# Kernel tuning notes

Measured on AMD Instinct MI355X. Metric: run time of the kernel, lower is better.

The kernel has to match this reference:

```python
import jax, jax.numpy as jnp
import numpy as np

HID = 256  # hidden_dim in the torch module


def _graph_conv(h, edges, W0, b0, W1, b1):
    # pytorch3d.ops.GraphConv (undirected): out = w0(h) + sum_{neighbors} w1(h_nbr),
    # where each edge (i, j) contributes in both directions.
    out = h @ W0 + b0          # [V, H]
    nbr = h @ W1 + b1          # [V, H]
    i, j = edges[:, 0], edges[:, 1]
    out = out.at[i].add(nbr[j])
    out = out.at[j].add(nbr[i])
    return out


def setup_inputs() -> dict:
    key = jax.random.key(0)
    ks = jax.random.split(key, 16)
    V, E, F, H = 20496, 61440, 3840, HID  # 8 meshes x (2562 verts, 7680 edges); F = 256+512+1024+2048

    def w(k, shape):
        return jax.random.normal(k, shape, dtype=jnp.float32) * 0.02

    return {
        "vert_img_feats": jax.random.normal(ks[0], (V, F), dtype=jnp.float32),
        "verts": jax.random.normal(ks[1], (V, 3), dtype=jnp.float32),
        "edges": jax.random.randint(ks[2], (E, 2), 0, V),
        # bottleneck Linear(3840 -> 256)
        "Wb": w(ks[3], (F, H)), "bb": jnp.zeros((H,), jnp.float32),
        # GraphConv 0: input_dim = 3 + 256
        "W0_0": w(ks[4], (3 + H, H)), "b0_0": jnp.zeros((H,), jnp.float32),
        "W1_0": w(ks[5], (3 + H, H)), "b1_0": jnp.zeros((H,), jnp.float32),
        # GraphConv 1..9 stacked
        "gW0": w(ks[6], (9, H, H)), "gb0": jnp.zeros((9, H), jnp.float32),
        "gW1": w(ks[7], (9, H, H)), "gb1": jnp.zeros((9, H), jnp.float32),
        # vert_offset Linear(256 -> 3)
        "Wo": w(ks[8], (H, 3)), "bo": jnp.zeros((3,), jnp.float32),
        # asym_conf MLP: 256 -> 256 -> 64 -> 32 -> 1
        "A1": w(ks[9], (H, H)), "a1": jnp.zeros((H,), jnp.float32),
        "A2": w(ks[10], (H, 64)), "a2": jnp.zeros((64,), jnp.float32),
        "A3": w(ks[11], (64, 32)), "a3": jnp.zeros((32,), jnp.float32),
        "A4": w(ks[12], (32, 1)), "a4": jnp.zeros((1,), jnp.float32),
    }


def reference(vert_img_feats, verts, edges, Wb, bb, W0_0, b0_0, W1_0, b1_0,
              gW0, gb0, gW1, gb1, Wo, bo, A1, a1, A2, a2, A3, a3, A4, a4):
    # bottleneck + ReLU on per-vertex image features (vert_align output)
    h_img = jax.nn.relu(vert_img_feats @ Wb + bb)            # [V, 256]
    h = jnp.concatenate([h_img, verts], axis=1)              # [V, 259]
    h = jax.nn.relu(_graph_conv(h, edges, W0_0, b0_0, W1_0, b1_0))
    for k in range(9):  # fixed layer count, structurally distinct params
        h = jax.nn.relu(_graph_conv(h, edges, gW0[k], gb0[k], gW1[k], gb1[k]))
    delta_v = h @ Wo + bo                                    # [V, 3]
    z = jax.nn.relu(h @ A1 + a1)
    z = jax.nn.relu(z @ A2 + a2)
    z = jax.nn.relu(z @ A3 + a3)
    asym_conf = jax.nn.sigmoid(z @ A4 + a4)                  # [V, 1]
    return delta_v, asym_conf
```

## Files before the change

kernel.cpp:

```cpp
#include <hip/hip_runtime.h>

typedef _Float16 half8  __attribute__((ext_vector_type(8)));
typedef _Float16 half4v __attribute__((ext_vector_type(4)));
typedef float    floatx4 __attribute__((ext_vector_type(4)));

#define DEVINL __device__ __forceinline__

DEVINL void async_cp16(const void* g, void* l){
  __builtin_amdgcn_global_load_lds(
      (const __attribute__((address_space(1))) void*)g,
      (__attribute__((address_space(3))) void*)l,
      16, 0, 0);
}

DEVINL float wred64(float x){
  #pragma unroll
  for (int m = 32; m; m >>= 1) x += __shfl_xor(x, m, 64);
  return x;
}

__global__ __launch_bounds__(256) void k_gemm_bb(
    const float* __restrict__ A, const _Float16* __restrict__ BT,
    const float* __restrict__ bias, _Float16* __restrict__ C,
    int M, int K, int lda)
{
  constexpr int BM = 128, BN = 128, BK = 32;
  __shared__ alignas(16) float    As[BM * BK];
  __shared__ alignas(16) _Float16 Bs[BN * BK];
  const int tid = threadIdx.x, wid = tid >> 6, lane = tid & 63;
  const int bm = blockIdx.x, bn = blockIdx.y;

  const float* aSrc[4]; float* aDst[4];
  const int uSw = (lane & 7) ^ ((lane >> 3) & 7);
  #pragma unroll
  for (int c = 0; c < 4; c++){
    int rloc = wid * 32 + c * 8 + (lane >> 3);
    int r = min(bm * BM + rloc, M - 1);
    aSrc[c] = A + (size_t)r * lda + uSw * 4;
    aDst[c] = &As[(wid * 32 + c * 8) * BK];
  }
  const _Float16* bSrc[2]; _Float16* bDst[2];
  #pragma unroll
  for (int s = 0; s < 2; s++){
    int rb = bn * BN + (wid * 2 + s) * 16 + (lane >> 2);
    bSrc[s] = BT + (size_t)rb * K + (lane & 3) * 8;
    bDst[s] = &Bs[(wid * 2 + s) * 16 * BK];
  }

  floatx4 acc[4][4];
  #pragma unroll
  for (int mt = 0; mt < 4; mt++)
    #pragma unroll
    for (int nt = 0; nt < 4; nt++) acc[mt][nt] = {0.f, 0.f, 0.f, 0.f};

  const int arow0 = (wid >> 1) * 64 + (lane & 15);
  const int g2 = (lane >> 4) * 2;
  const int boff = ((wid & 1) * 64 + (lane & 15)) * BK + (lane >> 4) * 8;

  for (int k0 = 0; k0 < K; k0 += BK){
    __syncthreads();
    #pragma unroll
    for (int c = 0; c < 4; c++) async_cp16(aSrc[c] + k0, aDst[c]);
    #pragma unroll
    for (int s = 0; s < 2; s++) async_cp16(bSrc[s] + k0, bDst[s]);
    __syncthreads();
    half8 af[4], bf[4];
    #pragma unroll
    for (int mt = 0; mt < 4; mt++){
      int arow = arow0 + mt * 16;
      int a7 = arow & 7;
      floatx4 lo = *(const floatx4*)&As[arow * BK + ((g2    ) ^ a7) * 4];
      floatx4 hi = *(const floatx4*)&As[arow * BK + ((g2 + 1) ^ a7) * 4];
      #pragma unroll
      for (int j = 0; j < 4; j++){ af[mt][j] = (_Float16)lo[j]; af[mt][4+j] = (_Float16)hi[j]; }
    }
    #pragma unroll
    for (int nt = 0; nt < 4; nt++) bf[nt] = *(const half8*)&Bs[boff + nt * 16 * BK];
    #pragma unroll
    for (int mt = 0; mt < 4; mt++)
      #pragma unroll
      for (int nt = 0; nt < 4; nt++)
        acc[mt][nt] = __builtin_amdgcn_mfma_f32_16x16x32_f16(af[mt], bf[nt], acc[mt][nt], 0, 0, 0);
  }

  const int colLocal = (wid & 1) * 64 + (lane & 15);
  const int rowLocal = (wid >> 1) * 64 + (lane >> 4) * 4;
  #pragma unroll
  for (int nt = 0; nt < 4; nt++){
    int col = bn * BN + colLocal + nt * 16;
    float b = bias[col];
    #pragma unroll
    for (int mt = 0; mt < 4; mt++){
      int r0 = bm * BM + rowLocal + mt * 16;
      #pragma unroll
      for (int i = 0; i < 4; i++){
        int r = r0 + i;
        if (r < M){
          float v = fmaxf(acc[mt][nt][i] + b, 0.f);
          C[(size_t)r * 256 + col] = (_Float16)v;
        }
      }
    }
  }
}

template<bool RELU, bool SPLIT, bool VERTC>
__global__ __launch_bounds__(256) void k_gemm_h(
    const _Float16* __restrict__ A, int Mstore, int Vreal,
    const _Float16* __restrict__ BT,
    const float* __restrict__ bias0, const float* __restrict__ bias1,
    const float* __restrict__ vertW, const float* __restrict__ verts,
    _Float16* __restrict__ C0, _Float16* __restrict__ C1)
{
  constexpr int BM = 128, BN = 128, BK = 32, K = 256;
  __shared__ alignas(16) _Float16 As[BM * BK];
  __shared__ alignas(16) _Float16 Bs[BN * BK];
  const int tid = threadIdx.x, wid = tid >> 6, lane = tid & 63;
  const int bm = blockIdx.x, bn = blockIdx.y;
  const int sub = lane >> 2, kof = (lane & 3) * 8;

  const _Float16* aSrc[2]; _Float16* aDst[2];
  const _Float16* bSrc[2]; _Float16* bDst[2];
  #pragma unroll
  for (int s = 0; s < 2; s++){
    int r = bm * BM + (wid * 2 + s) * 16 + sub;
    aSrc[s] = A + (size_t)r * K + kof;
    aDst[s] = &As[(wid * 2 + s) * 512];
    int rb = bn * BN + (wid * 2 + s) * 16 + sub;
    bSrc[s] = BT + (size_t)rb * K + kof;
    bDst[s] = &Bs[(wid * 2 + s) * 512];
  }

  floatx4 acc[4][4];
  #pragma unroll
  for (int mt = 0; mt < 4; mt++)
    #pragma unroll
    for (int nt = 0; nt < 4; nt++) acc[mt][nt] = {0.f, 0.f, 0.f, 0.f};

  const int aoff = ((wid >> 1) * 64 + (lane & 15)) * BK + (lane >> 4) * 8;
  const int boff = ((wid & 1) * 64 + (lane & 15)) * BK + (lane >> 4) * 8;

  for (int k0 = 0; k0 < K; k0 += BK){
    __syncthreads();
    async_cp16(aSrc[0] + k0, aDst[0]);
    async_cp16(aSrc[1] + k0, aDst[1]);
    async_cp16(bSrc[0] + k0, bDst[0]);
    async_cp16(bSrc[1] + k0, bDst[1]);
    __syncthreads();
    half8 af[4], bf[4];
    #pragma unroll
    for (int mt = 0; mt < 4; mt++) af[mt] = *(const half8*)&As[aoff + mt * 16 * BK];
    #pragma unroll
    for (int nt = 0; nt < 4; nt++) bf[nt] = *(const half8*)&Bs[boff + nt * 16 * BK];
    #pragma unroll
    for (int mt = 0; mt < 4; mt++)
      #pragma unroll
      for (int nt = 0; nt < 4; nt++)
        acc[mt][nt] = __builtin_amdgcn_mfma_f32_16x16x32_f16(af[mt], bf[nt], acc[mt][nt], 0, 0, 0);
  }

  const int colLocal = (wid & 1) * 64 + (lane & 15);
  const int rowLocal = (wid >> 1) * 64 + (lane >> 4) * 4;
  #pragma unroll
  for (int nt = 0; nt < 4; nt++){
    int g = bn * BN + colLocal + nt * 16;
    _Float16* Cp = C0;
    const float* bp = bias0;
    int col = g;
    if (SPLIT && g >= 256){ Cp = C1; bp = bias1; col = g - 256; }
    float b = bp[col];
    float w0 = 0.f, w1 = 0.f, w2 = 0.f;
    if (VERTC){ w0 = vertW[g*3+0]; w1 = vertW[g*3+1]; w2 = vertW[g*3+2]; }
    #pragma unroll
    for (int mt = 0; mt < 4; mt++){
      int r0 = bm * BM + rowLocal + mt * 16;
      #pragma unroll
      for (int i = 0; i < 4; i++){
        int r = r0 + i;
        if (r < Mstore){
          float v = acc[mt][nt][i] + b;
          if (VERTC){
            int vr = min(r, Vreal - 1);
            v += verts[vr*3+0] * w0 + verts[vr*3+1] * w1 + verts[vr*3+2] * w2;
          }
          if (RELU) v = fmaxf(v, 0.f);
          Cp[(size_t)r * 256 + col] = (_Float16)v;
        }
      }
    }
  }
}

__global__ __launch_bounds__(256) void k_fill(const int* __restrict__ e, int E,
                                              int* __restrict__ cnt, int* __restrict__ adj){
  int t = blockIdx.x * 256 + threadIdx.x;
  if (t >= E) return;
  int i = e[t*2], j = e[t*2+1];
  int s = atomicAdd(&cnt[i], 1); if (s < 64) adj[(size_t)i*64 + s] = j;
  int q = atomicAdd(&cnt[j], 1); if (q < 64) adj[(size_t)j*64 + q] = i;
}

__global__ __launch_bounds__(256) void k_pack(
    const float* __restrict__ Wb,
    const float* __restrict__ W0_0, const float* __restrict__ W1_0,
    const float* __restrict__ gW0,  const float* __restrict__ gW1,
    const float* __restrict__ A1,
    _Float16* __restrict__ WbT, _Float16* __restrict__ convB,
    _Float16* __restrict__ A1T, float* __restrict__ vertW)
{
  const int S1 = 256*3840, S2 = 10*512*256, S3 = 256*256, S4 = 512*3;
  int id = blockIdx.x * 256 + threadIdx.x;
  if (id < S1){ int n = id / 3840, k = id % 3840; WbT[id] = (_Float16)Wb[(size_t)k*256 + n]; return; }
  id -= S1;
  if (id < S2){
    int l = id / (512*256); int rem = id % (512*256);
    int r = rem / 256, k = rem % 256;
    const float* W0 = (l == 0) ? W0_0 : gW0 + (size_t)(l-1)*65536;
    const float* W1 = (l == 0) ? W1_0 : gW1 + (size_t)(l-1)*65536;
    convB[id] = (_Float16)((r < 256) ? W0[(size_t)k*256 + r] : W1[(size_t)k*256 + (r-256)]);
    return;
  }
  id -= S2;
  if (id < S3){ int n = id / 256, k = id % 256; A1T[id] = (_Float16)A1[(size_t)k*256 + n]; return; }
  id -= S3;
  if (id < S4){
    int n = id / 3, c = id % 3;
    vertW[id] = (n < 256) ? W0_0[(size_t)(256+c)*256 + n]
                          : W1_0[(size_t)(256+c)*256 + (n-256)];
  }
}

__global__ __launch_bounds__(256) void k_gather(
    const _Float16* __restrict__ outB, const _Float16* __restrict__ nbrB,
    const int* __restrict__ cnt, const int* __restrict__ adj,
    _Float16* __restrict__ h, int V)
{
  int gw = (int)((blockIdx.x * 256 + threadIdx.x) >> 6);
  int lane = threadIdx.x & 63;
  if (gw >= V) return;
  half4v o = ((const half4v*)(outB + (size_t)gw * 256))[lane];
  float a0 = (float)o[0], a1 = (float)o[1], a2 = (float)o[2], a3 = (float)o[3];
  int n = min(cnt[gw], 64);
  const int* ap = adj + (size_t)gw * 64;
  for (int d = 0; d < n; d++){
    int u = ap[d];
    half4v x = ((const half4v*)(nbrB + (size_t)u * 256))[lane];
    a0 += (float)x[0]; a1 += (float)x[1]; a2 += (float)x[2]; a3 += (float)x[3];
  }
  half4v rr;
  rr[0] = (_Float16)fmaxf(a0, 0.f); rr[1] = (_Float16)fmaxf(a1, 0.f);
  rr[2] = (_Float16)fmaxf(a2, 0.f); rr[3] = (_Float16)fmaxf(a3, 0.f);
  ((half4v*)(h + (size_t)gw * 256))[lane] = rr;
}

__global__ __launch_bounds__(1024) void k_head(
    const _Float16* __restrict__ hA, const _Float16* __restrict__ z1,
    const float* __restrict__ Wo, const float* __restrict__ bo,
    const float* __restrict__ A2, const float* __restrict__ a2,
    const float* __restrict__ A3, const float* __restrict__ a3,
    const float* __restrict__ A4, const float* __restrict__ a4,
    float* __restrict__ dOut, int V)
{
  __shared__ float A2s[256 * 64];
  __shared__ float A3s[64 * 32];
  __shared__ float Wos[768];
  __shared__ float zrow[16][256];
  __shared__ float z2s[16][64];
  const int tid = threadIdx.x;
  for (int i = tid; i < 256*64; i += 1024) A2s[i] = A2[i];
  for (int i = tid; i < 64*32;  i += 1024) A3s[i] = A3[i];
  if (tid < 768) Wos[tid] = Wo[tid];
  __syncthreads();
  const int wid = tid >> 6, lane = tid & 63;
  const int v = blockIdx.x * 16 + wid;
  if (v >= V) return;

  half4v hv = ((const half4v*)(hA + (size_t)v * 256))[lane];
  float hf[4] = { (float)hv[0], (float)hv[1], (float)hv[2], (float)hv[3] };
  float p0 = 0.f, p1 = 0.f, p2 = 0.f;
  int c0 = lane * 4;
  #pragma unroll
  for (int j = 0; j < 4; j++){
    p0 += hf[j] * Wos[(c0+j)*3 + 0];
    p1 += hf[j] * Wos[(c0+j)*3 + 1];
    p2 += hf[j] * Wos[(c0+j)*3 + 2];
  }
  p0 = wred64(p0); p1 = wred64(p1); p2 = wred64(p2);
  if (lane == 0){
    dOut[(size_t)v*3 + 0] = p0 + bo[0];
    dOut[(size_t)v*3 + 1] = p1 + bo[1];
    dOut[(size_t)v*3 + 2] = p2 + bo[2];
  }

  half4v zv = ((const half4v*)(z1 + (size_t)v * 256))[lane];
  floatx4 zf; zf[0] = (float)zv[0]; zf[1] = (float)zv[1]; zf[2] = (float)zv[2]; zf[3] = (float)zv[3];
  ((floatx4*)zrow[wid])[lane] = zf;
  __threadfence_block();
  float acc2 = a2[lane];
  #pragma unroll 4
  for (int c = 0; c < 256; c++) acc2 += zrow[wid][c] * A2s[c*64 + lane];
  acc2 = fmaxf(acc2, 0.f);
  z2s[wid][lane] = acc2;
  __threadfence_block();
  int o = lane & 31;
  float acc3 = a3[o];
  #pragma unroll 4
  for (int c = 0; c < 64; c++) acc3 += z2s[wid][c] * A3s[c*32 + o];
  acc3 = fmaxf(acc3, 0.f);
  float p = (lane < 32) ? acc3 * A4[lane] : 0.f;
  p = wred64(p);
  if (lane == 0){
    float s = 1.f / (1.f + expf(-(p + a4[0])));
    dOut[(size_t)V*3 + v] = s;
  }
}

extern "C" void kernel_launch(void* const* d_in, const int* in_sizes, int n_in,
                              void* d_out, int out_size, void* d_ws, size_t ws_size,
                              hipStream_t stream)
{
  const int V = 20496, E = 61440, F = 3840, Vpad = 20608;
  const float* X     = (const float*)d_in[0];
  const float* verts = (const float*)d_in[1];
  const int*   edges = (const int*)d_in[2];
  const float* Wb    = (const float*)d_in[3];
  const float* bb    = (const float*)d_in[4];
  const float* W0_0  = (const float*)d_in[5];
  const float* b0_0  = (const float*)d_in[6];
  const float* W1_0  = (const float*)d_in[7];
  const float* b1_0  = (const float*)d_in[8];
  const float* gW0   = (const float*)d_in[9];
  const float* gb0   = (const float*)d_in[10];
  const float* gW1   = (const float*)d_in[11];
  const float* gb1   = (const float*)d_in[12];
  const float* Wo    = (const float*)d_in[13];
  const float* bo    = (const float*)d_in[14];
  const float* A1    = (const float*)d_in[15];
  const float* a1    = (const float*)d_in[16];
  const float* A2    = (const float*)d_in[17];
  const float* a2    = (const float*)d_in[18];
  const float* A3    = (const float*)d_in[19];
  const float* a3    = (const float*)d_in[20];
  const float* A4    = (const float*)d_in[21];
  const float* a4    = (const float*)d_in[22];

  char* w = (char*)d_ws;
  const size_t SA = (size_t)Vpad * 256 * 2;
  _Float16* hA    = (_Float16*)(w);
  _Float16* outB  = (_Float16*)(w + SA);
  _Float16* nbrB  = (_Float16*)(w + 2*SA);
  _Float16* z1    = (_Float16*)(w + 3*SA);
  size_t off = 4 * SA;
  _Float16* WbT   = (_Float16*)(w + off); off += (size_t)256*3840*2;
  _Float16* convB = (_Float16*)(w + off); off += (size_t)10*512*256*2;
  _Float16* A1T   = (_Float16*)(w + off); off += (size_t)256*256*2;
  float*    vertW = (float*)(w + off);    off += (size_t)512*3*4;
  int*      cnt   = (int*)(w + off);      off += (size_t)V*4;
  int*      adj   = (int*)(w + off);

  hipMemsetAsync(cnt, 0, (size_t)V*4, stream);
  hipMemsetAsync(hA + (size_t)V*256, 0, (size_t)(Vpad - V)*256*2, stream);

  k_fill<<<dim3((E + 255)/256), dim3(256), 0, stream>>>(edges, E, cnt, adj);
  {
    const int total = 256*3840 + 10*512*256 + 256*256 + 512*3;
    k_pack<<<dim3((total + 255)/256), dim3(256), 0, stream>>>(
        Wb, W0_0, W1_0, gW0, gW1, A1, WbT, convB, A1T, vertW);
  }

  k_gemm_bb<<<dim3(161, 2), dim3(256), 0, stream>>>(X, WbT, bb, hA, V, F, F);

  for (int l = 0; l < 10; l++){
    const float* bp0 = l ? gb0 + (size_t)(l-1)*256 : b0_0;
    const float* bp1 = l ? gb1 + (size_t)(l-1)*256 : b1_0;
    const _Float16* Bt = convB + (size_t)l * 512 * 256;
    if (l == 0)
      k_gemm_h<false, true, true><<<dim3(161, 4), dim3(256), 0, stream>>>(
          hA, Vpad, V, Bt, bp0, bp1, vertW, verts, outB, nbrB);
    else
      k_gemm_h<false, true, false><<<dim3(161, 4), dim3(256), 0, stream>>>(
          hA, Vpad, V, Bt, bp0, bp1, nullptr, nullptr, outB, nbrB);
    k_gather<<<dim3(5124), dim3(256), 0, stream>>>(outB, nbrB, cnt, adj, hA, V);
  }

  k_gemm_h<true, false, false><<<dim3(161, 2), dim3(256), 0, stream>>>(
      hA, Vpad, V, A1T, a1, nullptr, nullptr, nullptr, z1, nullptr);

  k_head<<<dim3(V/16), dim3(1024), 0, stream>>>(
      hA, z1, Wo, bo, A2, a2, A3, a3, A4, a4, (float*)d_out, V);
}
```

Before: 1.070 ms.

## Split-K bottleneck GEMM, fragment-packed conv weights, tiled transpose, unrolled gather

The bottleneck GEMM is split along K into four chunks that write fp32 partials, and a separate reduce kernel adds bias, applies ReLU and zeroes the padding rows. This raises parallelism above the 322 blocks the grid had before. Conv and head GEMMs now preload a whole 128-column weight panel, packed into MFMA fragment order, into LDS once, and read A straight from global memory, which removes the per-K-step barriers. Weight packing is split into a tiled LDS transpose and a fragment packer, and the neighbor gather loop is unrolled by two. The cost is extra fp32 partial traffic and 64KB of LDS per block, which can lower occupancy.

```diff
diff --git a/kernel.cpp b/kernel.cpp
--- a/kernel.cpp
+++ b/kernel.cpp
@@ -21,29 +21,30 @@
 
 __global__ __launch_bounds__(256) void k_gemm_bb(
     const float* __restrict__ A, const _Float16* __restrict__ BT,
-    const float* __restrict__ bias, _Float16* __restrict__ C,
-    int M, int K, int lda)
-{
-  constexpr int BM = 128, BN = 128, BK = 32;
+    float* __restrict__ P, int M, int Mpad, int K, int lda, int kChunk)
+{
+  constexpr int BM = 128, BK = 32;
   __shared__ alignas(16) float    As[BM * BK];
-  __shared__ alignas(16) _Float16 Bs[BN * BK];
+  __shared__ alignas(16) _Float16 Bs[BM * BK];
   const int tid = threadIdx.x, wid = tid >> 6, lane = tid & 63;
-  const int bm = blockIdx.x, bn = blockIdx.y;
+  const int bm = blockIdx.x, bn = blockIdx.y, bz = blockIdx.z;
+  const int kbeg = bz * kChunk, kend = kbeg + kChunk;
 
   const float* aSrc[4]; float* aDst[4];
-  const int uSw = (lane & 7) ^ ((lane >> 3) & 7);
+  const int uSwA = (lane & 7) ^ ((lane >> 3) & 7);
   #pragma unroll
   for (int c = 0; c < 4; c++){
     int rloc = wid * 32 + c * 8 + (lane >> 3);
     int r = min(bm * BM + rloc, M - 1);
-    aSrc[c] = A + (size_t)r * lda + uSw * 4;
+    aSrc[c] = A + (size_t)r * lda + uSwA * 4;
     aDst[c] = &As[(wid * 32 + c * 8) * BK];
   }
   const _Float16* bSrc[2]; _Float16* bDst[2];
+  const int uSwB = (lane & 3) ^ ((lane >> 2) & 3);
   #pragma unroll
   for (int s = 0; s < 2; s++){
-    int rb = bn * BN + (wid * 2 + s) * 16 + (lane >> 2);
-    bSrc[s] = BT + (size_t)rb * K + (lane & 3) * 8;
+    int rb = bn * BM + (wid * 2 + s) * 16 + (lane >> 2);
+    bSrc[s] = BT + (size_t)rb * K + uSwB * 8;
     bDst[s] = &Bs[(wid * 2 + s) * 16 * BK];
   }
 
@@ -55,9 +56,11 @@
 
   const int arow0 = (wid >> 1) * 64 + (lane & 15);
   const int g2 = (lane >> 4) * 2;
-  const int boff = ((wid & 1) * 64 + (lane & 15)) * BK + (lane >> 4) * 8;
-
-  for (int k0 = 0; k0 < K; k0 += BK){
+  const int a7 = lane & 7;
+  const int brow0 = (wid & 1) * 64 + (lane & 15);
+  const int ub = (lane >> 4) ^ (lane & 3);
+
+  for (int k0 = kbeg; k0 < kend; k0 += BK){
     __syncthreads();
     #pragma unroll
     for (int c = 0; c < 4; c++) async_cp16(aSrc[c] + k0, aDst[c]);
@@ -68,14 +71,14 @@
     #pragma unroll
     for (int mt = 0; mt < 4; mt++){
       int arow = arow0 + mt * 16;
-      int a7 = arow & 7;
       floatx4 lo = *(const floatx4*)&As[arow * BK + ((g2    ) ^ a7) * 4];
       floatx4 hi = *(const floatx4*)&As[arow * BK + ((g2 + 1) ^ a7) * 4];
       #pragma unroll
       for (int j = 0; j < 4; j++){ af[mt][j] = (_Float16)lo[j]; af[mt][4+j] = (_Float16)hi[j]; }
     }
     #pragma unroll
-    for (int nt = 0; nt < 4; nt++) bf[nt] = *(const half8*)&Bs[boff + nt * 16 * BK];
+    for (int nt = 0; nt < 4; nt++)
+      bf[nt] = *(const half8*)&Bs[(brow0 + nt * 16) * BK + ub * 8];
     #pragma unroll
     for (int mt = 0; mt < 4; mt++)
       #pragma unroll
@@ -85,51 +88,72 @@
 
   const int colLocal = (wid & 1) * 64 + (lane & 15);
   const int rowLocal = (wid >> 1) * 64 + (lane >> 4) * 4;
+  float* Pz = P + (size_t)bz * Mpad * 256;
   #pragma unroll
   for (int nt = 0; nt < 4; nt++){
-    int col = bn * BN + colLocal + nt * 16;
-    float b = bias[col];
+    int col = bn * BM + colLocal + nt * 16;
     #pragma unroll
     for (int mt = 0; mt < 4; mt++){
       int r0 = bm * BM + rowLocal + mt * 16;
       #pragma unroll
-      for (int i = 0; i < 4; i++){
-        int r = r0 + i;
-        if (r < M){
-          float v = fmaxf(acc[mt][nt][i] + b, 0.f);
-          C[(size_t)r * 256 + col] = (_Float16)v;
-        }
-      }
+      for (int i = 0; i < 4; i++)
+        Pz[(size_t)(r0 + i) * 256 + col] = acc[mt][nt][i];
     }
   }
 }
 
+__global__ __launch_bounds__(256) void k_reduce(
+    const float* __restrict__ P, const float* __restrict__ bias,
+    _Float16* __restrict__ hA, int V, int Mpad)
+{
+  int idx = blockIdx.x * 256 + threadIdx.x;
+  int base = idx * 4;
+  int r = base >> 8, c = base & 255;
+  const size_t stride = (size_t)Mpad * 256;
+  const float* p = P + (size_t)r * 256 + c;
+  floatx4 s0 = *(const floatx4*)(p);
+  floatx4 s1 = *(const floatx4*)(p + stride);
+  floatx4 s2 = *(const floatx4*)(p + 2 * stride);
+  floatx4 s3 = *(const floatx4*)(p + 3 * stride);
+  floatx4 b = *(const floatx4*)(bias + c);
+  half4v o;
+  if (r < V){
+    #pragma unroll
+    for (int e = 0; e < 4; e++)
+      o[e] = (_Float16)fmaxf(s0[e] + s1[e] + s2[e] + s3[e] + b[e], 0.f);
+  } else {
+    #pragma unroll
+    for (int e = 0; e < 4; e++) o[e] = (_Float16)0.f;
+  }
+  *(half4v*)(hA + (size_t)r * 256 + c) = o;
+}
+
 template<bool RELU, bool SPLIT, bool VERTC>
-__global__ __launch_bounds__(256) void k_gemm_h(
-    const _Float16* __restrict__ A, int Mstore, int Vreal,
-    const _Float16* __restrict__ BT,
+__global__ __launch_bounds__(256) void k_conv(
+    const _Float16* __restrict__ A,
+    const _Float16* __restrict__ BTfrag,
     const float* __restrict__ bias0, const float* __restrict__ bias1,
     const float* __restrict__ vertW, const float* __restrict__ verts,
-    _Float16* __restrict__ C0, _Float16* __restrict__ C1)
-{
-  constexpr int BM = 128, BN = 128, BK = 32, K = 256;
-  __shared__ alignas(16) _Float16 As[BM * BK];
-  __shared__ alignas(16) _Float16 Bs[BN * BK];
+    _Float16* __restrict__ C0, _Float16* __restrict__ C1, int Vreal)
+{
+  __shared__ alignas(16) _Float16 Bs[32768];
   const int tid = threadIdx.x, wid = tid >> 6, lane = tid & 63;
   const int bm = blockIdx.x, bn = blockIdx.y;
-  const int sub = lane >> 2, kof = (lane & 3) * 8;
-
-  const _Float16* aSrc[2]; _Float16* aDst[2];
-  const _Float16* bSrc[2]; _Float16* bDst[2];
-  #pragma unroll
-  for (int s = 0; s < 2; s++){
-    int r = bm * BM + (wid * 2 + s) * 16 + sub;
-    aSrc[s] = A + (size_t)r * K + kof;
-    aDst[s] = &As[(wid * 2 + s) * 512];
-    int rb = bn * BN + (wid * 2 + s) * 16 + sub;
-    bSrc[s] = BT + (size_t)rb * K + kof;
-    bDst[s] = &Bs[(wid * 2 + s) * 512];
-  }
+
+  const _Float16* src = BTfrag + (size_t)bn * 32768;
+  #pragma unroll
+  for (int jj = 0; jj < 16; jj++){
+    int e = (jj * 256 + tid) * 8;
+    *(half8*)&Bs[e] = *(const half8*)&src[e];
+  }
+  __syncthreads();
+
+  const _Float16* Arow[4];
+  #pragma unroll
+  for (int mt = 0; mt < 4; mt++)
+    Arow[mt] = A + (size_t)(bm * 128 + (wid >> 1) * 64 + mt * 16 + (lane & 15)) * 256
+                 + (lane >> 4) * 8;
+  const int nbase = (wid & 1) * 4;
 
   floatx4 acc[4][4];
   #pragma unroll
@@ -137,21 +161,14 @@
     #pragma unroll
     for (int nt = 0; nt < 4; nt++) acc[mt][nt] = {0.f, 0.f, 0.f, 0.f};
 
-  const int aoff = ((wid >> 1) * 64 + (lane & 15)) * BK + (lane >> 4) * 8;
-  const int boff = ((wid & 1) * 64 + (lane & 15)) * BK + (lane >> 4) * 8;
-
-  for (int k0 = 0; k0 < K; k0 += BK){
-    __syncthreads();
-    async_cp16(aSrc[0] + k0, aDst[0]);
-    async_cp16(aSrc[1] + k0, aDst[1]);
-    async_cp16(bSrc[0] + k0, bDst[0]);
-    async_cp16(bSrc[1] + k0, bDst[1]);
-    __syncthreads();
+  #pragma unroll
+  for (int j = 0; j < 8; j++){
     half8 af[4], bf[4];
     #pragma unroll
-    for (int mt = 0; mt < 4; mt++) af[mt] = *(const half8*)&As[aoff + mt * 16 * BK];
-    #pragma unroll
-    for (int nt = 0; nt < 4; nt++) bf[nt] = *(const half8*)&Bs[boff + nt * 16 * BK];
+    for (int mt = 0; mt < 4; mt++) af[mt] = *(const half8*)(Arow[mt] + j * 32);
+    #pragma unroll
+    for (int nt = 0; nt < 4; nt++)
+      bf[nt] = *(const half8*)&Bs[(((nbase + nt) * 8 + j) * 64 + lane) * 8];
     #pragma unroll
     for (int mt = 0; mt < 4; mt++)
       #pragma unroll
@@ -163,7 +180,7 @@
   const int rowLocal = (wid >> 1) * 64 + (lane >> 4) * 4;
   #pragma unroll
   for (int nt = 0; nt < 4; nt++){
-    int g = bn * BN + colLocal + nt * 16;
+    int g = bn * 128 + colLocal + nt * 16;
     _Float16* Cp = C0;
     const float* bp = bias0;
     int col = g;
@@ -173,19 +190,17 @@
     if (VERTC){ w0 = vertW[g*3+0]; w1 = vertW[g*3+1]; w2 = vertW[g*3+2]; }
     #pragma unroll
     for (int mt = 0; mt < 4; mt++){
-      int r0 = bm * BM + rowLocal + mt * 16;
+      int r0 = bm * 128 + rowLocal + mt * 16;
       #pragma unroll
       for (int i = 0; i < 4; i++){
         int r = r0 + i;
-        if (r < Mstore){
-          float v = acc[mt][nt][i] + b;
-          if (VERTC){
-            int vr = min(r, Vreal - 1);
-            v += verts[vr*3+0] * w0 + verts[vr*3+1] * w1 + verts[vr*3+2] * w2;
-          }
-          if (RELU) v = fmaxf(v, 0.f);
-          Cp[(size_t)r * 256 + col] = (_Float16)v;
+        float v = acc[mt][nt][i] + b;
+        if (VERTC){
+          int vr = min(r, Vreal - 1);
+          v += verts[vr*3+0] * w0 + verts[vr*3+1] * w1 + verts[vr*3+2] * w2;
         }
+        if (RELU) v = fmaxf(v, 0.f);
+        Cp[(size_t)r * 256 + col] = (_Float16)v;
       }
     }
   }
@@ -200,33 +215,63 @@
   int q = atomicAdd(&cnt[j], 1); if (q < 64) adj[(size_t)j*64 + q] = i;
 }
 
-__global__ __launch_bounds__(256) void k_pack(
-    const float* __restrict__ Wb,
+__global__ __launch_bounds__(256) void k_trans_bb(
+    const float* __restrict__ Wb, _Float16* __restrict__ WbT)
+{
+  __shared__ float T[64][65];
+  const int k0 = blockIdx.x * 64, n0 = blockIdx.y * 64;
+  const int tr = threadIdx.x >> 6, tc = threadIdx.x & 63;
+  #pragma unroll
+  for (int i = 0; i < 16; i++){
+    int rr = i * 4 + tr;
+    T[rr][tc] = Wb[(size_t)(k0 + rr) * 256 + n0 + tc];
+  }
+  __syncthreads();
+  #pragma unroll
+  for (int i = 0; i < 16; i++){
+    int rr = i * 4 + tr;
+    WbT[(size_t)(n0 + rr) * 3840 + k0 + tc] = (_Float16)T[tc][rr];
+  }
+}
+
+__global__ __launch_bounds__(256) void k_pack_frag(
     const float* __restrict__ W0_0, const float* __restrict__ W1_0,
     const float* __restrict__ gW0,  const float* __restrict__ gW1,
     const float* __restrict__ A1,
-    _Float16* __restrict__ WbT, _Float16* __restrict__ convB,
-    _Float16* __restrict__ A1T, float* __restrict__ vertW)
-{
-  const int S1 = 256*3840, S2 = 10*512*256, S3 = 256*256, S4 = 512*3;
-  int id = blockIdx.x * 256 + threadIdx.x;
-  if (id < S1){ int n = id / 3840, k = id % 3840; WbT[id] = (_Float16)Wb[(size_t)k*256 + n]; return; }
-  id -= S1;
-  if (id < S2){
-    int l = id / (512*256); int rem = id % (512*256);
-    int r = rem / 256, k = rem % 256;
-    const float* W0 = (l == 0) ? W0_0 : gW0 + (size_t)(l-1)*65536;
-    const float* W1 = (l == 0) ? W1_0 : gW1 + (size_t)(l-1)*65536;
-    convB[id] = (_Float16)((r < 256) ? W0[(size_t)k*256 + r] : W1[(size_t)k*256 + (r-256)]);
+    _Float16* __restrict__ convB, _Float16* __restrict__ A1T,
+    float* __restrict__ vertW)
+{
+  if (blockIdx.x == 672){
+    for (int i = threadIdx.x; i < 1536; i += 256){
+      int n = i / 3, c = i % 3;
+      vertW[i] = (n < 256) ? W0_0[(size_t)(256 + c) * 256 + n]
+                           : W1_0[(size_t)(256 + c) * 256 + (n - 256)];
+    }
     return;
   }
-  id -= S2;
-  if (id < S3){ int n = id / 256, k = id % 256; A1T[id] = (_Float16)A1[(size_t)k*256 + n]; return; }
-  id -= S3;
-  if (id < S4){
-    int n = id / 3, c = id % 3;
-    vertW[id] = (n < 256) ? W0_0[(size_t)(256+c)*256 + n]
-                          : W1_0[(size_t)(256+c)*256 + (n-256)];
+  const int gw = blockIdx.x * 4 + (threadIdx.x >> 6);
+  const int lane = threadIdx.x & 63;
+  if (gw < 2560){
+    int L = gw >> 8;
+    int r = gw & 255;
+    int n = (r >> 3) * 16 + (lane & 15);
+    int k = (r & 7) * 32 + (lane >> 4) * 8;
+    const float* W0 = L ? gW0 + (size_t)(L - 1) * 65536 : W0_0;
+    const float* W1 = L ? gW1 + (size_t)(L - 1) * 65536 : W1_0;
+    const float* Wsel = (n < 256) ? W0 : W1;
+    int nn = n & 255;
+    half8 v;
+    #pragma unroll
+    for (int e = 0; e < 8; e++) v[e] = (_Float16)Wsel[(size_t)(k + e) * 256 + nn];
+    *(half8*)&convB[(size_t)L * 131072 + (size_t)r * 512 + lane * 8] = v;
+  } else {
+    int r = gw - 2560;
+    int n = (r >> 3) * 16 + (lane & 15);
+    int k = (r & 7) * 32 + (lane >> 4) * 8;
+    half8 v;
+    #pragma unroll
+    for (int e = 0; e < 8; e++) v[e] = (_Float16)A1[(size_t)(k + e) * 256 + n];
+    *(half8*)&A1T[(size_t)r * 512 + lane * 8] = v;
   }
 }
 
@@ -242,7 +287,15 @@
   float a0 = (float)o[0], a1 = (float)o[1], a2 = (float)o[2], a3 = (float)o[3];
   int n = min(cnt[gw], 64);
   const int* ap = adj + (size_t)gw * 64;
-  for (int d = 0; d < n; d++){
+  int d = 0;
+  for (; d + 1 < n; d += 2){
+    int u0 = ap[d], u1 = ap[d+1];
+    half4v x = ((const half4v*)(nbrB + (size_t)u0 * 256))[lane];
+    half4v y = ((const half4v*)(nbrB + (size_t)u1 * 256))[lane];
+    a0 += (float)x[0] + (float)y[0]; a1 += (float)x[1] + (float)y[1];
+    a2 += (float)x[2] + (float)y[2]; a3 += (float)x[3] + (float)y[3];
+  }
+  if (d < n){
     int u = ap[d];
     half4v x = ((const half4v*)(nbrB + (size_t)u * 256))[lane];
     a0 += (float)x[0]; a1 += (float)x[1]; a2 += (float)x[2]; a3 += (float)x[3];
@@ -324,7 +377,7 @@
   const float* verts = (const float*)d_in[1];
   const int*   edges = (const int*)d_in[2];
   const float* Wb    = (const float*)d_in[3];
-  const float* bb    = (const float*)d_in[4];
+  const float* bbias = (const float*)d_in[4];
   const float* W0_0  = (const float*)d_in[5];
   const float* b0_0  = (const float*)d_in[6];
   const float* W1_0  = (const float*)d_in[7];
@@ -351,40 +404,39 @@
   _Float16* nbrB  = (_Float16*)(w + 2*SA);
   _Float16* z1    = (_Float16*)(w + 3*SA);
   size_t off = 4 * SA;
+  float*    P     = (float*)(w + off);    off += (size_t)4 * Vpad * 256 * 4;
   _Float16* WbT   = (_Float16*)(w + off); off += (size_t)256*3840*2;
-  _Float16* convB = (_Float16*)(w + off); off += (size_t)10*512*256*2;
-  _Float16* A1T   = (_Float16*)(w + off); off += (size_t)256*256*2;
-  float*    vertW = (float*)(w + off);    off += (size_t)512*3*4;
+  _Float16* convB = (_Float16*)(w + off); off += (size_t)10*131072*2;
+  _Float16* A1T   = (_Float16*)(w + off); off += (size_t)131072*2;
+  float*    vertW = (float*)(w + off);    off += (size_t)1536*4;
   int*      cnt   = (int*)(w + off);      off += (size_t)V*4;
   int*      adj   = (int*)(w + off);
 
   hipMemsetAsync(cnt, 0, (size_t)V*4, stream);
-  hipMemsetAsync(hA + (size_t)V*256, 0, (size_t)(Vpad - V)*256*2, stream);
 
   k_fill<<<dim3((E + 255)/256), dim3(256), 0, stream>>>(edges, E, cnt, adj);
-  {
-    const int total = 256*3840 + 10*512*256 + 256*256 + 512*3;
-    k_pack<<<dim3((total + 255)/256), dim3(256), 0, stream>>>(
-        Wb, W0_0, W1_0, gW0, gW1, A1, WbT, convB, A1T, vertW);
-  }
-
-  k_gemm_bb<<<dim3(161, 2), dim3(256), 0, stream>>>(X, WbT, bb, hA, V, F, F);
+  k_trans_bb<<<dim3(60, 4), dim3(256), 0, stream>>>(Wb, WbT);
+  k_pack_frag<<<dim3(673), dim3(256), 0, stream>>>(
+      W0_0, W1_0, gW0, gW1, A1, convB, A1T, vertW);
+
+  k_gemm_bb<<<dim3(161, 2, 4), dim3(256), 0, stream>>>(X, WbT, P, V, Vpad, F, F, 960);
+  k_reduce<<<dim3(Vpad * 64 / 256), dim3(256), 0, stream>>>(P, bbias, hA, V, Vpad);
 
   for (int l = 0; l < 10; l++){
     const float* bp0 = l ? gb0 + (size_t)(l-1)*256 : b0_0;
     const float* bp1 = l ? gb1 + (size_t)(l-1)*256 : b1_0;
-    const _Float16* Bt = convB + (size_t)l * 512 * 256;
+    const _Float16* Bt = convB + (size_t)l * 131072;
     if (l == 0)
-      k_gemm_h<false, true, true><<<dim3(161, 4), dim3(256), 0, stream>>>(
-          hA, Vpad, V, Bt, bp0, bp1, vertW, verts, outB, nbrB);
+      k_conv<false, true, true><<<dim3(161, 4), dim3(256), 0, stream>>>(
+          hA, Bt, bp0, bp1, vertW, verts, outB, nbrB, V);
     else
-      k_gemm_h<false, true, false><<<dim3(161, 4), dim3(256), 0, stream>>>(
-          hA, Vpad, V, Bt, bp0, bp1, nullptr, nullptr, outB, nbrB);
+      k_conv<false, true, false><<<dim3(161, 4), dim3(256), 0, stream>>>(
+          hA, Bt, bp0, bp1, nullptr, nullptr, outB, nbrB, V);
     k_gather<<<dim3(5124), dim3(256), 0, stream>>>(outB, nbrB, cnt, adj, hA, V);
   }
 
-  k_gemm_h<true, false, false><<<dim3(161, 2), dim3(256), 0, stream>>>(
-      hA, Vpad, V, A1T, a1, nullptr, nullptr, nullptr, z1, nullptr);
+  k_conv<true, false, false><<<dim3(161, 2), dim3(256), 0, stream>>>(
+      hA, A1T, a1, nullptr, nullptr, nullptr, z1, nullptr, V);
 
   k_head<<<dim3(V/16), dim3(1024), 0, stream>>>(
       hA, z1, Wo, bo, A2, a2, A3, a3, A4, a4, (float*)d_out, V);
```

After: 991.6 us. -7.3%, faster.
